# Optimization experiments

Hardware: AMD Instinct MI355X
Metric: run time of the kernel (lower is better)

## Reference

```python
import jax, jax.numpy as jnp
import numpy as np

N_HEADS = 8
TOP_K = 2
EPS = 1e-5


def cross_node(x4, nf, tkv, Wq, bq, Wk, bk, Wv, bv, Wo, bo, gamma, beta, token_mask):
    # x4: [N, BL, 1, D]; nf: [N, BL, K, D]; tkv: [N, K, 1]; token_mask: [N] float (routed subset)
    N, BL, _, D = x4.shape
    K = nf.shape[2]
    H = N_HEADS
    dh = D // H
    nf = nf * tkv[:, None, :, :]  # use_weights: scale neighbors by topk similarity weights
    xf = x4.reshape(N * BL, D)
    nff = nf.reshape(N * BL, K, D)
    q = (xf @ Wq.T + bq).reshape(N * BL, H, dh)
    k = (nff @ Wk.T + bk).reshape(N * BL, K, H, dh)
    v = (nff @ Wv.T + bv).reshape(N * BL, K, H, dh)
    # flash_attn_func math: scaled dot-product over the K neighbors, per head
    scores = jnp.einsum('thd,tkhd->thk', q, k) / jnp.sqrt(jnp.asarray(dh, xf.dtype))
    attn = jax.nn.softmax(scores, axis=-1)
    o = jnp.einsum('thk,tkhd->thd', attn, v).reshape(N * BL, D)
    o = o @ Wo.T + bo
    # masked BatchNorm1d (training-mode batch stats over ONLY the gathered/routed tokens,
    # matching torch where each expert sees just its subset)
    m = jnp.broadcast_to(token_mask[:, None], (N, BL)).reshape(-1, 1)
    cnt = jnp.maximum(m.sum(), 1.0)
    mean = (o * m).sum(0) / cnt
    var = (((o - mean) ** 2) * m).sum(0) / cnt
    o = (o - mean) / jnp.sqrt(var + EPS) * gamma + beta
    return (o + xf).reshape(N, BL, D)


def moe_forward(x, mm, topk_values, Wr, br, eWq, eWk, eWv, eWo, ebq, ebk, ebv, ebo,
                eGamma, eBeta, eW1, eb1, mWq, mWk, mWv, mWo, mbq, mbk, mbv, mbo,
                mGamma, mBeta, mW2, mb2, topk_indices, modality_index):
    N, B, L, D = x.shape
    BL = B * L
    K = topk_indices.shape[1]
    E = Wr.shape[0]
    Mn = mWq.shape[0]
    # neighbor gather: nf[n, b*l, k] = x[topk_indices[n, k], b, l]
    nf = jnp.transpose(x[topk_indices], (0, 2, 3, 1, 4)).reshape(N, BL, K, D)
    x4 = x.reshape(N, BL, 1, D)
    tkv = topk_values.reshape(N, K, 1)
    # router softmax gating
    gate = jax.nn.softmax(mm.reshape(N, D) @ Wr.T + br, axis=-1)  # [N, E]
    _, te = jax.lax.top_k(gate, TOP_K)
    routed = jax.nn.one_hot(te, E, dtype=gate.dtype).sum(1)  # [N, E] 0/1
    f_i = routed.sum(0) / N
    P_i = gate.sum(0) / N
    balance_loss = E * jnp.sum(f_i * P_i)
    # capacity limiting via running cumsum per expert column
    keep = jnp.cumsum(routed, axis=0) <= (N / E)
    rprobs = gate * jnp.where(keep, routed, jnp.zeros_like(routed))
    active = rprobs.sum(-1) > 0  # [N]
    eprobs, eidx = jax.lax.top_k(rprobs, TOP_K)  # [N, TOP_K]
    # expert dispatch/combine (dense-masked equivalent of the per-expert gather/scatter)
    out_tok = jnp.zeros((N, BL, D), x.dtype)
    for i in range(E):
        sel = (eidx == i).any(-1) & active  # tokens gathered for expert i
        mask_f = sel.astype(x.dtype)
        prob_i = (eprobs * (eidx == i)).sum(-1)  # combine weight (0 for capacity-dropped)
        co = cross_node(x4, nf, tkv, eWq[i], ebq[i], eWk[i], ebk[i], eWv[i], ebv[i],
                        eWo[i], ebo[i], eGamma[i], eBeta[i], mask_f)
        co = co @ eW1[i].T + eb1[i]
        out_tok = out_tok + (mask_f * prob_i)[:, None, None] * co
    # modality experts: every token with modality m goes through modality expert m
    mod_out = jnp.zeros_like(out_tok)
    for m in range(Mn):
        mask_f = (modality_index[:, m, :] == 1).any(-1).astype(x.dtype)
        co = cross_node(x4, nf, tkv, mWq[m], mbq[m], mWk[m], mbk[m], mWv[m], mbv[m],
                        mWo[m], mbo[m], mGamma[m], mBeta[m], mask_f)
        co = co @ mW2[m].T + mb2[m]
        mod_out = mod_out + mask_f[:, None, None] * co
    out = (out_tok + mod_out / Mn).reshape(N, B, L, D)
    return out, balance_loss


def setup_inputs():
    key = jax.random.key(0)
    ks = jax.random.split(key, 7)
    N, B, L, D, K, E, Mn = 1024, 2, 8, 128, 16, 4, 4
    s = 1.0 / float(np.sqrt(D))
    inp = {}
    inp['x'] = jax.random.normal(ks[0], (N, B, L, D), jnp.float32)
    inp['mm'] = jax.random.normal(ks[1], (N, 1, D), jnp.float32)
    inp['topk_values'] = jax.random.uniform(ks[2], (N, K), jnp.float32)
    inp['topk_indices'] = jax.random.randint(ks[3], (N, K), 0, N, dtype=jnp.int32)
    inp['modality_index'] = jax.nn.one_hot(
        jax.random.randint(ks[4], (N,), 0, Mn, dtype=jnp.int32), Mn, dtype=jnp.int32
    ).reshape(N, Mn, 1)
    inp['Wr'] = jax.random.normal(ks[5], (E, D), jnp.float32) * s
    inp['br'] = jnp.zeros((E,), jnp.float32)
    kk = jax.random.split(ks[6], 10)
    for j, nm in enumerate(['eWq', 'eWk', 'eWv', 'eWo', 'eW1']):
        inp[nm] = jax.random.normal(kk[j], (E, D, D), jnp.float32) * s
    for j, nm in enumerate(['mWq', 'mWk', 'mWv', 'mWo', 'mW2']):
        inp[nm] = jax.random.normal(kk[5 + j], (Mn, D, D), jnp.float32) * s
    for nm in ['ebq', 'ebk', 'ebv', 'ebo', 'eBeta', 'eb1']:
        inp[nm] = jnp.zeros((E, D), jnp.float32)
    for nm in ['mbq', 'mbk', 'mbv', 'mbo', 'mBeta', 'mb2']:
        inp[nm] = jnp.zeros((Mn, D), jnp.float32)
    inp['eGamma'] = jnp.ones((E, D), jnp.float32)
    inp['mGamma'] = jnp.ones((Mn, D), jnp.float32)
    return inp


def reference(x, mm, topk_values, topk_indices, modality_index, Wr, br,
              eWq, eWk, eWv, eWo, ebq, ebk, ebv, ebo, eGamma, eBeta, eW1, eb1,
              mWq, mWk, mWv, mWo, mbq, mbk, mbv, mbo, mGamma, mBeta, mW2, mb2):
    return moe_forward(x, mm, topk_values, Wr, br, eWq, eWk, eWv, eWo, ebq, ebk, ebv, ebo,
                       eGamma, eBeta, eW1, eb1, mWq, mWk, mWv, mWo, mbq, mbk, mbv, mbo,
                       mGamma, mBeta, mW2, mb2, topk_indices, modality_index)
```

## Files before the change

kernel.cpp:

```cpp
#include <hip/hip_runtime.h>

typedef unsigned short u16;
typedef unsigned int u32;
typedef short short8 __attribute__((ext_vector_type(8)));
typedef float f32x4 __attribute__((ext_vector_type(4)));

#define NTOK 1024
#define TT 16384
#define DD 128
#define EPSV 1e-5f
#define ST 2097152
#define STKV 4194304

__device__ __forceinline__ u16 f2bf(float f) {
    u32 u = __float_as_uint(f);
    u += 0x7fffu + ((u >> 16) & 1u);
    return (u16)(u >> 16);
}
__device__ __forceinline__ u32 pack2(u16 a, u16 b) { return (u32)a | ((u32)b << 16); }
__device__ __forceinline__ void up2(u32 w, float& lo, float& hi) {
    lo = __uint_as_float(w << 16);
    hi = __uint_as_float(w & 0xffff0000u);
}

__global__ __launch_bounds__(1024) void k_prep(const float* __restrict__ x,
        const float* __restrict__ eWq, const float* __restrict__ eWk,
        const float* __restrict__ eWv, const float* __restrict__ eWo, const float* __restrict__ eW1,
        const float* __restrict__ mWq, const float* __restrict__ mWk, const float* __restrict__ mWv,
        const float* __restrict__ mWo, const float* __restrict__ mW2,
        const float* __restrict__ mm, const float* __restrict__ Wr, const float* __restrict__ br,
        const int* __restrict__ modix,
        u16* __restrict__ Xb, u16* __restrict__ Wb,
        float* __restrict__ mask8, float* __restrict__ comb8, float* __restrict__ cnt8,
        float* __restrict__ bnsum, float* __restrict__ bnsq, float* __restrict__ loss) {
    int bid = blockIdx.x; int tid = threadIdx.x;
    if (bid < 256) {
        int i = bid * 1024 + tid;
        const float4* p = (const float4*)x + (size_t)i * 2;
        float4 a = p[0], b = p[1];
        uint4 o;
        o.x = pack2(f2bf(a.x), f2bf(a.y));
        o.y = pack2(f2bf(a.z), f2bf(a.w));
        o.z = pack2(f2bf(b.x), f2bf(b.y));
        o.w = pack2(f2bf(b.z), f2bf(b.w));
        *((uint4*)Xb + i) = o;
        return;
    }
    if (bid < 336) {
        int i = (bid - 256) * 1024 + tid;
        int tns = i >> 13;
        int off = (i & 8191) * 8;
        const float* src;
        switch (tns) {
            case 0: src = eWq; break; case 1: src = eWk; break; case 2: src = eWv; break;
            case 3: src = eWo; break; case 4: src = eW1; break; case 5: src = mWq; break;
            case 6: src = mWk; break; case 7: src = mWv; break; case 8: src = mWo; break;
            default: src = mW2; break;
        }
        const float4* p = (const float4*)(src + off);
        float4 a = p[0], b = p[1];
        uint4 o;
        o.x = pack2(f2bf(a.x), f2bf(a.y));
        o.y = pack2(f2bf(a.z), f2bf(a.w));
        o.z = pack2(f2bf(b.x), f2bf(b.y));
        o.w = pack2(f2bf(b.z), f2bf(b.w));
        *(uint4*)(Wb + tns * 65536 + off) = o;
        return;
    }
    __shared__ int wsum[4][16];
    __shared__ float red[16];
    int n = tid;
    if (n < 16) red[n] = 0.f;
    bnsum[n] = 0.f; bnsq[n] = 0.f;
    float g[4];
    {
        const float4* a = (const float4*)(mm + (size_t)n * DD);
        float4 av[32];
#pragma unroll
        for (int j = 0; j < 32; j++) av[j] = a[j];
#pragma unroll
        for (int e = 0; e < 4; e++) {
            const float4* w = (const float4*)(Wr + (size_t)e * DD);
            float s = 0.f;
#pragma unroll
            for (int j = 0; j < 32; j++) {
                float4 wv = w[j];
                s += av[j].x * wv.x + av[j].y * wv.y + av[j].z * wv.z + av[j].w * wv.w;
            }
            g[e] = s + br[e];
        }
    }
    float mx = -1e30f;
#pragma unroll
    for (int e = 0; e < 4; e++) mx = fmaxf(mx, g[e]);
    float s = 0.f;
#pragma unroll
    for (int e = 0; e < 4; e++) { g[e] = expf(g[e] - mx); s += g[e]; }
    float inv = 1.f / s;
#pragma unroll
    for (int e = 0; e < 4; e++) g[e] *= inv;
    int i0 = 0; float b0 = g[0];
#pragma unroll
    for (int e = 1; e < 4; e++) if (g[e] > b0) { b0 = g[e]; i0 = e; }
    int i1 = -1; float b1v = -1e30f;
#pragma unroll
    for (int e = 0; e < 4; e++) if (e != i0 && g[e] > b1v) { b1v = g[e]; i1 = e; }
    u32 rbits = (1u << i0) | (1u << i1);
    int wav = n >> 6, lane = n & 63;
    unsigned long long lm = (~0ull) >> (63 - lane);
    int pre[4];
#pragma unroll
    for (int e = 0; e < 4; e++) {
        unsigned long long m = __ballot((rbits >> e) & 1u);
        pre[e] = __popcll(m & lm);
        if (lane == 63) wsum[e][wav] = __popcll(m);
    }
    __syncthreads();
    float rp[4]; float rsum = 0.f;
#pragma unroll
    for (int e = 0; e < 4; e++) {
        int off = 0;
        for (int w = 0; w < 16; w++) if (w < wav) off += wsum[e][w];
        bool keep = (off + pre[e]) <= 256;
        rp[e] = (((rbits >> e) & 1u) && keep) ? g[e] : 0.f;
        rsum += rp[e];
    }
    bool active = rsum > 0.f;
    int j0 = 0; float c0 = rp[0];
#pragma unroll
    for (int e = 1; e < 4; e++) if (rp[e] > c0) { c0 = rp[e]; j0 = e; }
    int j1 = -1; float c1 = -1e30f;
#pragma unroll
    for (int e = 0; e < 4; e++) if (e != j0 && rp[e] > c1) { c1 = rp[e]; j1 = e; }
    float vals[16];
#pragma unroll
    for (int e = 0; e < 4; e++) {
        bool sel = active && (e == j0 || e == j1);
        float mf = sel ? 1.f : 0.f;
        mask8[e * NTOK + n] = mf;
        comb8[e * NTOK + n] = rp[e];
        vals[e] = mf;
    }
#pragma unroll
    for (int m = 0; m < 4; m++) {
        float mf = (modix[n * 4 + m] == 1) ? 1.f : 0.f;
        mask8[(4 + m) * NTOK + n] = mf;
        comb8[(4 + m) * NTOK + n] = 0.25f * mf;
        vals[4 + m] = mf;
    }
#pragma unroll
    for (int e = 0; e < 4; e++) vals[8 + e] = ((rbits >> e) & 1u) ? 1.f : 0.f;
#pragma unroll
    for (int e = 0; e < 4; e++) vals[12 + e] = g[e];
#pragma unroll
    for (int q = 0; q < 16; q++) {
        float v = vals[q];
        for (int off = 32; off; off >>= 1) v += __shfl_down(v, off, 64);
        if (lane == 0) atomicAdd(&red[q], v);
    }
    __syncthreads();
    if (n == 0) {
        for (int c = 0; c < 8; c++) cnt8[c] = fmaxf(16.f * red[c], 1.f);
        float l = 0.f;
        for (int e = 0; e < 4; e++) l += (red[8 + e] / 1024.f) * (red[12 + e] / 1024.f);
        loss[0] = 4.f * l;
    }
}

__global__ __launch_bounds__(256) void k_gemm_qkv(const u16* __restrict__ Xb, const u16* __restrict__ Wb,
        const float* __restrict__ ebq, const float* __restrict__ mbq,
        const float* __restrict__ mask8,
        u16* __restrict__ Qb, u16* __restrict__ KVb) {
    __shared__ u16 As[64 * 128];
    __shared__ u16 Bs[128 * 128];
    int tid = threadIdx.x; int bm = blockIdx.x; int c = blockIdx.y;
    int wq = (c < 4) ? c : 20 + (c - 4);
    int wk = (c < 4) ? 4 + c : 24 + (c - 4);
    int wv = (c < 4) ? 8 + c : 28 + (c - 4);
    const u16* Wsl[3] = { Wb + wq * 16384, Wb + wk * 16384, Wb + wv * 16384 };
    const float* bq = (c < 4) ? (ebq + c * 128) : (mbq + (c - 4) * 128);
    const float* maskp = mask8 + c * NTOK;
    bool qact = (maskp[bm * 4] != 0.f) || (maskp[bm * 4 + 1] != 0.f) ||
                (maskp[bm * 4 + 2] != 0.f) || (maskp[bm * 4 + 3] != 0.f);
    u16* Qc  = Qb + (size_t)c * ST;
    u16* KVc = KVb + (size_t)c * STKV;

    const uint4* asrc = (const uint4*)(Xb + (size_t)bm * 8192);
#pragma unroll
    for (int it = 0; it < 4; ++it) {
        int ci = it * 256 + tid;
        uint4 v = asrc[ci];
        int byte = ci * 16; int row = byte >> 8;
        *(uint4*)((char*)As + (byte ^ ((row & 7) << 4))) = v;
    }
    __syncthreads();
    int lane = tid & 63, wid = tid >> 6, lr = lane & 15, lg = lane >> 4;
    short8 a[4];
#pragma unroll
    for (int ks = 0; ks < 4; ++ks) {
        int kk = ks * 64 + lg * 16;
        int arow = wid * 16 + lr;
        a[ks] = *(const short8*)((const char*)As + ((arow * 256 + kk) ^ ((arow & 7) << 4)));
    }
    for (int y = 0; y < 3; ++y) {
        if (y == 0 && !qact) continue;
        const uint4* wsrc = (const uint4*)Wsl[y];
#pragma unroll
        for (int it = 0; it < 8; ++it) {
            int qi = it * 256 + tid;
            uint4 v = wsrc[qi];
            int eo = qi * 8; int row = eo >> 7; int byte = eo * 2;
            *(uint4*)((char*)Bs + (byte ^ ((row & 7) << 4))) = v;
        }
        __syncthreads();
        f32x4 acc[8] = {};
#pragma unroll
        for (int ks = 0; ks < 4; ++ks) {
            int kk = ks * 64 + lg * 16;
#pragma unroll
            for (int nc = 0; nc < 8; ++nc) {
                int brow = nc * 16 + lr;
                short8 b = *(const short8*)((const char*)Bs + ((brow * 256 + kk) ^ ((brow & 7) << 4)));
                acc[nc] = __builtin_amdgcn_mfma_f32_16x16x32_bf16(a[ks], b, acc[nc], 0, 0, 0);
            }
        }
        int row0 = bm * 64 + wid * 16 + lg * 4;
#pragma unroll
        for (int nc = 0; nc < 8; ++nc) {
            int col = nc * 16 + lr;
            float bb = (y == 0) ? bq[col] : 0.f;
#pragma unroll
            for (int r = 0; r < 4; r++) {
                u16 hv = f2bf(acc[nc][r] + bb);
                if (y == 0) Qc[(size_t)(row0 + r) * 128 + col] = hv;
                else KVc[(size_t)(row0 + r) * 256 + (y == 2 ? 128 : 0) + col] = hv;
            }
        }
        __syncthreads();
    }
}

__global__ __launch_bounds__(256) void k_attn(const u16* Qb, const u16* __restrict__ KVb,
        const float* __restrict__ tkv, const int* __restrict__ idx,
        const float* __restrict__ ebk, const float* __restrict__ ebv,
        const float* __restrict__ mbk, const float* __restrict__ mbv,
        const float* __restrict__ mask8, u16* Ob) {
    int bid = blockIdx.x;
    int c = bid & 7, inner = bid >> 3;
    int tid = threadIdx.x;
    int gid = inner * 256 + tid;
    int t = gid >> 3, h = gid & 7;
    int n = __builtin_amdgcn_readfirstlane(t >> 4);
    int bl = t & 15;
    if (mask8[c * NTOK + n] == 0.f) return;
    const int4* ip = (const int4*)(idx + n * 16);
    int4 iv0 = ip[0], iv1 = ip[1], iv2 = ip[2], iv3 = ip[3];
    const float4* tp = (const float4*)(tkv + n * 16);
    float4 tv0 = tp[0], tv1 = tp[1], tv2 = tp[2], tv3 = tp[3];
    const u16* Qc = Qb + (size_t)c * ST;
    const u16* KVc = KVb + (size_t)c * STKV;
    u16* Oc = Ob + (size_t)c * ST;
    const float* bk = (c < 4) ? (ebk + c * 128) : (mbk + (c - 4) * 128);
    const float* bv = (c < 4) ? (ebv + c * 128) : (mbv + (c - 4) * 128);
    float qv[16];
    {
        const uint4* qp = (const uint4*)(Qc + (size_t)t * 128 + h * 16);
        uint4 a = qp[0], b = qp[1];
        up2(a.x, qv[0], qv[1]);   up2(a.y, qv[2], qv[3]);
        up2(a.z, qv[4], qv[5]);   up2(a.w, qv[6], qv[7]);
        up2(b.x, qv[8], qv[9]);   up2(b.y, qv[10], qv[11]);
        up2(b.z, qv[12], qv[13]); up2(b.w, qv[14], qv[15]);
    }
    float qb = 0.f;
#pragma unroll
    for (int i = 0; i < 16; i++) qb += qv[i] * bk[h * 16 + i];
    int gsav[16] = { iv0.x, iv0.y, iv0.z, iv0.w, iv1.x, iv1.y, iv1.z, iv1.w,
                     iv2.x, iv2.y, iv2.z, iv2.w, iv3.x, iv3.y, iv3.z, iv3.w };
    float tsav[16] = { tv0.x, tv0.y, tv0.z, tv0.w, tv1.x, tv1.y, tv1.z, tv1.w,
                       tv2.x, tv2.y, tv2.z, tv2.w, tv3.x, tv3.y, tv3.z, tv3.w };
    float scv[16]; float smax = -1e30f;
#pragma unroll 4
    for (int k = 0; k < 16; k++) {
        const uint4* kp = (const uint4*)(KVc + (size_t)(gsav[k] * 16 + bl) * 256 + h * 16);
        uint4 a = kp[0], b = kp[1];
        float d0 = 0.f, d1 = 0.f, lo, hi;
        up2(a.x, lo, hi); d0 = fmaf(lo, qv[0], d0);  d1 = fmaf(hi, qv[1], d1);
        up2(a.y, lo, hi); d0 = fmaf(lo, qv[2], d0);  d1 = fmaf(hi, qv[3], d1);
        up2(a.z, lo, hi); d0 = fmaf(lo, qv[4], d0);  d1 = fmaf(hi, qv[5], d1);
        up2(a.w, lo, hi); d0 = fmaf(lo, qv[6], d0);  d1 = fmaf(hi, qv[7], d1);
        up2(b.x, lo, hi); d0 = fmaf(lo, qv[8], d0);  d1 = fmaf(hi, qv[9], d1);
        up2(b.y, lo, hi); d0 = fmaf(lo, qv[10], d0); d1 = fmaf(hi, qv[11], d1);
        up2(b.z, lo, hi); d0 = fmaf(lo, qv[12], d0); d1 = fmaf(hi, qv[13], d1);
        up2(b.w, lo, hi); d0 = fmaf(lo, qv[14], d0); d1 = fmaf(hi, qv[15], d1);
        float sv = 0.25f * (tsav[k] * (d0 + d1) + qb);
        scv[k] = sv; smax = fmaxf(smax, sv);
    }
    float sum = 0.f;
#pragma unroll
    for (int k = 0; k < 16; k++) { scv[k] = __expf(scv[k] - smax); sum += scv[k]; }
    float inv = 1.f / sum;
    float o[16];
#pragma unroll
    for (int i = 0; i < 16; i++) o[i] = 0.f;
#pragma unroll 4
    for (int k = 0; k < 16; k++) {
        const uint4* vp = (const uint4*)(KVc + (size_t)(gsav[k] * 16 + bl) * 256 + 128 + h * 16);
        uint4 a = vp[0], b = vp[1];
        float cc = scv[k] * inv * tsav[k];
        float lo, hi;
        up2(a.x, lo, hi); o[0] = fmaf(lo, cc, o[0]);   o[1] = fmaf(hi, cc, o[1]);
        up2(a.y, lo, hi); o[2] = fmaf(lo, cc, o[2]);   o[3] = fmaf(hi, cc, o[3]);
        up2(a.z, lo, hi); o[4] = fmaf(lo, cc, o[4]);   o[5] = fmaf(hi, cc, o[5]);
        up2(a.w, lo, hi); o[6] = fmaf(lo, cc, o[6]);   o[7] = fmaf(hi, cc, o[7]);
        up2(b.x, lo, hi); o[8] = fmaf(lo, cc, o[8]);   o[9] = fmaf(hi, cc, o[9]);
        up2(b.y, lo, hi); o[10] = fmaf(lo, cc, o[10]); o[11] = fmaf(hi, cc, o[11]);
        up2(b.z, lo, hi); o[12] = fmaf(lo, cc, o[12]); o[13] = fmaf(hi, cc, o[13]);
        up2(b.w, lo, hi); o[14] = fmaf(lo, cc, o[14]); o[15] = fmaf(hi, cc, o[15]);
    }
#pragma unroll
    for (int i = 0; i < 16; i++) o[i] += bv[h * 16 + i];
    uint4 s0, s1;
    s0.x = pack2(f2bf(o[0]), f2bf(o[1]));  s0.y = pack2(f2bf(o[2]), f2bf(o[3]));
    s0.z = pack2(f2bf(o[4]), f2bf(o[5]));  s0.w = pack2(f2bf(o[6]), f2bf(o[7]));
    s1.x = pack2(f2bf(o[8]), f2bf(o[9]));  s1.y = pack2(f2bf(o[10]), f2bf(o[11]));
    s1.z = pack2(f2bf(o[12]), f2bf(o[13])); s1.w = pack2(f2bf(o[14]), f2bf(o[15]));
    uint4* op = (uint4*)(Oc + (size_t)t * 128 + h * 16);
    op[0] = s0; op[1] = s1;
}

__global__ __launch_bounds__(256) void k_gemm_o(const u16* __restrict__ Ab, const u16* __restrict__ Wb,
        const float* __restrict__ ebo, const float* __restrict__ mbo,
        u16* __restrict__ O2, const float* __restrict__ mask8,
        float* __restrict__ bnsum, float* __restrict__ bnsq) {
    __shared__ u16 As[64 * 128];
    __shared__ u16 Bs[128 * 128];
    __shared__ float ssum[128], ssq[128];
    int tid = threadIdx.x; int bm = blockIdx.x; int c = blockIdx.y;
    const float* maskp = mask8 + c * NTOK;
    if (maskp[bm * 4] == 0.f && maskp[bm * 4 + 1] == 0.f &&
        maskp[bm * 4 + 2] == 0.f && maskp[bm * 4 + 3] == 0.f) return;
    int wo = (c < 4) ? 12 + c : 32 + (c - 4);
    const u16* Wp = Wb + wo * 16384;
    const float* bo = (c < 4) ? (ebo + c * 128) : (mbo + (c - 4) * 128);
    if (tid < 128) { ssum[tid] = 0.f; ssq[tid] = 0.f; }
    const uint4* asrc = (const uint4*)(Ab + (size_t)c * ST + (size_t)bm * 8192);
#pragma unroll
    for (int it = 0; it < 4; ++it) {
        int ci = it * 256 + tid;
        uint4 v = asrc[ci];
        int byte = ci * 16; int row = byte >> 8;
        *(uint4*)((char*)As + (byte ^ ((row & 7) << 4))) = v;
    }
    const uint4* wsrc = (const uint4*)Wp;
#pragma unroll
    for (int it = 0; it < 8; ++it) {
        int qi = it * 256 + tid;
        uint4 v = wsrc[qi];
        int eo = qi * 8; int row = eo >> 7; int byte = eo * 2;
        *(uint4*)((char*)Bs + (byte ^ ((row & 7) << 4))) = v;
    }
    __syncthreads();
    int lane = tid & 63, wid = tid >> 6, lr = lane & 15, lg = lane >> 4;
    f32x4 acc[8] = {};
#pragma unroll
    for (int ks = 0; ks < 4; ++ks) {
        int kk = ks * 64 + lg * 16;
        int arow = wid * 16 + lr;
        short8 a = *(const short8*)((const char*)As + ((arow * 256 + kk) ^ ((arow & 7) << 4)));
#pragma unroll
        for (int nc = 0; nc < 8; ++nc) {
            int brow = nc * 16 + lr;
            short8 b = *(const short8*)((const char*)Bs + ((brow * 256 + kk) ^ ((brow & 7) << 4)));
            acc[nc] = __builtin_amdgcn_mfma_f32_16x16x32_bf16(a, b, acc[nc], 0, 0, 0);
        }
    }
    int nidx = bm * 4 + wid;
    float mk = maskp[nidx];
    int row0 = bm * 64 + wid * 16 + lg * 4;
    u16* O2c = O2 + (size_t)c * ST;
    float ps[8], pq[8];
#pragma unroll
    for (int nc = 0; nc < 8; ++nc) {
        int col = nc * 16 + lr;
        float bb = bo[col];
        float sv = 0.f, qv = 0.f;
#pragma unroll
        for (int r = 0; r < 4; r++) {
            float v = acc[nc][r] + bb;
            if (mk != 0.f) O2c[(size_t)(row0 + r) * 128 + col] = f2bf(v);
            sv += v; qv += v * v;
        }
        ps[nc] = sv * mk; pq[nc] = qv * mk;
    }
#pragma unroll
    for (int nc = 0; nc < 8; ++nc) {
        ps[nc] += __shfl_xor(ps[nc], 16, 64); ps[nc] += __shfl_xor(ps[nc], 32, 64);
        pq[nc] += __shfl_xor(pq[nc], 16, 64); pq[nc] += __shfl_xor(pq[nc], 32, 64);
    }
    if (lane < 16) {
#pragma unroll
        for (int nc = 0; nc < 8; ++nc) {
            atomicAdd(&ssum[nc * 16 + lane], ps[nc]);
            atomicAdd(&ssq[nc * 16 + lane], pq[nc]);
        }
    }
    __syncthreads();
    if (tid < 128) { atomicAdd(&bnsum[c * 128 + tid], ssum[tid]); atomicAdd(&bnsq[c * 128 + tid], ssq[tid]); }
}

__global__ __launch_bounds__(512) void k_gemm_w1(const u16* __restrict__ O2, const u16* __restrict__ Xb,
        const u16* __restrict__ Wb, const float* __restrict__ eb1, const float* __restrict__ mb2,
        const float* __restrict__ eGamma, const float* __restrict__ mGamma,
        const float* __restrict__ eBeta, const float* __restrict__ mBeta,
        const float* __restrict__ comb8, const float* __restrict__ cnt8,
        const float* __restrict__ bnsum, const float* __restrict__ bnsq,
        float* __restrict__ out) {
    __shared__ u16 As[64 * 128];
    __shared__ u16 Bs[128 * 128];
    __shared__ float scall[8][128], shall[8][128];
    int tid = threadIdx.x; int bm = blockIdx.x;
#pragma unroll
    for (int j = 0; j < 2; ++j) {
        int id = j * 512 + tid;
        int c = id >> 7, d = id & 127;
        float cnt = cnt8[c];
        float mean = bnsum[c * 128 + d] / cnt;
        float var = bnsq[c * 128 + d] / cnt - mean * mean;
        float rs = rsqrtf(var + EPSV);
        const float* ga = (c < 4) ? (eGamma + c * 128) : (mGamma + (c - 4) * 128);
        const float* be = (c < 4) ? (eBeta + c * 128) : (mBeta + (c - 4) * 128);
        float gg = ga[d];
        scall[c][d] = rs * gg;
        shall[c][d] = be[d] - mean * rs * gg;
    }
    __syncthreads();
    int lane = tid & 63, wid = tid >> 6, lr = lane & 15, lg = lane >> 4;
    int wm = wid & 3, wn = wid >> 2;
    f32x4 acc[4] = {};
    const uint4* xsrc = (const uint4*)(Xb + (size_t)bm * 8192);
    for (int c = 0; c < 8; ++c) {
        float wc4[4];
        wc4[0] = comb8[c * NTOK + bm * 4];     wc4[1] = comb8[c * NTOK + bm * 4 + 1];
        wc4[2] = comb8[c * NTOK + bm * 4 + 2]; wc4[3] = comb8[c * NTOK + bm * 4 + 3];
        if (wc4[0] == 0.f && wc4[1] == 0.f && wc4[2] == 0.f && wc4[3] == 0.f) continue;
        int wsl = (c < 4) ? 16 + c : 36 + (c - 4);
        const u16* Wp = Wb + wsl * 16384;
        const uint4* osrc = (const uint4*)(O2 + (size_t)c * ST + (size_t)bm * 8192);
#pragma unroll
        for (int it = 0; it < 2; ++it) {
            int qi = it * 512 + tid;
            int eo = qi * 8; int row = eo >> 7; int cb = eo & 127;
            float wc = wc4[row >> 4];
            uint4 ov = osrc[qi]; uint4 xv = xsrc[qi];
            float olo, ohi, xlo, xhi;
            uint4 hh;
            up2(ov.x, olo, ohi); up2(xv.x, xlo, xhi);
            hh.x = pack2(f2bf((olo * scall[c][cb] + shall[c][cb] + xlo) * wc),
                         f2bf((ohi * scall[c][cb + 1] + shall[c][cb + 1] + xhi) * wc));
            up2(ov.y, olo, ohi); up2(xv.y, xlo, xhi);
            hh.y = pack2(f2bf((olo * scall[c][cb + 2] + shall[c][cb + 2] + xlo) * wc),
                         f2bf((ohi * scall[c][cb + 3] + shall[c][cb + 3] + xhi) * wc));
            up2(ov.z, olo, ohi); up2(xv.z, xlo, xhi);
            hh.z = pack2(f2bf((olo * scall[c][cb + 4] + shall[c][cb + 4] + xlo) * wc),
                         f2bf((ohi * scall[c][cb + 5] + shall[c][cb + 5] + xhi) * wc));
            up2(ov.w, olo, ohi); up2(xv.w, xlo, xhi);
            hh.w = pack2(f2bf((olo * scall[c][cb + 6] + shall[c][cb + 6] + xlo) * wc),
                         f2bf((ohi * scall[c][cb + 7] + shall[c][cb + 7] + xhi) * wc));
            *(uint4*)((char*)As + ((eo * 2) ^ ((row & 7) << 4))) = hh;
        }
        const uint4* wsrc = (const uint4*)Wp;
#pragma unroll
        for (int it = 0; it < 4; ++it) {
            int qi = it * 512 + tid;
            uint4 v = wsrc[qi];
            int eo = qi * 8; int row = eo >> 7; int byte = eo * 2;
            *(uint4*)((char*)Bs + (byte ^ ((row & 7) << 4))) = v;
        }
        __syncthreads();
#pragma unroll
        for (int ks = 0; ks < 4; ++ks) {
            int kk = ks * 64 + lg * 16;
            int arow = wm * 16 + lr;
            short8 a = *(const short8*)((const char*)As + ((arow * 256 + kk) ^ ((arow & 7) << 4)));
#pragma unroll
            for (int nc = 0; nc < 4; ++nc) {
                int brow = wn * 64 + nc * 16 + lr;
                short8 b = *(const short8*)((const char*)Bs + ((brow * 256 + kk) ^ ((brow & 7) << 4)));
                acc[nc] = __builtin_amdgcn_mfma_f32_16x16x32_bf16(a, b, acc[nc], 0, 0, 0);
            }
        }
        __syncthreads();
    }
    int nidx = bm * 4 + wm;
    int row0 = bm * 64 + wm * 16 + lg * 4;
    float wc8[8];
#pragma unroll
    for (int c = 0; c < 8; ++c) wc8[c] = comb8[c * NTOK + nidx];
#pragma unroll
    for (int nc = 0; nc < 4; ++nc) {
        int col = wn * 64 + nc * 16 + lr;
        float bias = 0.f;
#pragma unroll
        for (int c = 0; c < 8; ++c) {
            const float* b1 = (c < 4) ? (eb1 + c * 128) : (mb2 + (c - 4) * 128);
            bias += wc8[c] * b1[col];
        }
#pragma unroll
        for (int r = 0; r < 4; r++)
            out[(size_t)(row0 + r) * 128 + col] = acc[nc][r] + bias;
    }
}

extern "C" void kernel_launch(void* const* d_in, const int* in_sizes, int n_in,
                              void* d_out, int out_size, void* d_ws, size_t ws_size,
                              hipStream_t stream) {
    (void)in_sizes; (void)n_in; (void)ws_size; (void)out_size;
    const float* x    = (const float*)d_in[0];
    const float* mm   = (const float*)d_in[1];
    const float* tkv  = (const float*)d_in[2];
    const int*   idx  = (const int*)d_in[3];
    const int*   modi = (const int*)d_in[4];
    const float* Wr   = (const float*)d_in[5];
    const float* br   = (const float*)d_in[6];
    const float* eWq = (const float*)d_in[7],  *eWk = (const float*)d_in[8],  *eWv = (const float*)d_in[9];
    const float* eWo = (const float*)d_in[10], *eW1 = (const float*)d_in[11];
    const float* mWq = (const float*)d_in[12], *mWk = (const float*)d_in[13], *mWv = (const float*)d_in[14];
    const float* mWo = (const float*)d_in[15], *mW2 = (const float*)d_in[16];
    const float* ebq = (const float*)d_in[17], *ebk = (const float*)d_in[18], *ebv = (const float*)d_in[19];
    const float* ebo = (const float*)d_in[20], *eBeta = (const float*)d_in[21], *eb1 = (const float*)d_in[22];
    const float* mbq = (const float*)d_in[23], *mbk = (const float*)d_in[24], *mbv = (const float*)d_in[25];
    const float* mbo = (const float*)d_in[26], *mBeta = (const float*)d_in[27], *mb2 = (const float*)d_in[28];
    const float* eGamma = (const float*)d_in[29], *mGamma = (const float*)d_in[30];
    float* out = (float*)d_out;

    char* wsb = (char*)d_ws;
    const size_t MB = 1024 * 1024;
    u16* Xb  = (u16*)wsb;
    u16* Wb  = (u16*)(wsb + 4 * MB);
    u16* Qb  = (u16*)(wsb + 8 * MB);
    u16* KVb = (u16*)(wsb + 40 * MB);
    u16* O2  = (u16*)(wsb + 104 * MB);
    float* comb8 = (float*)(wsb + 136 * MB);
    float* mask8 = comb8 + 8192;
    float* cnt8  = mask8 + 8192;
    float* bnsum = cnt8 + 16;
    float* bnsq  = bnsum + 1024;

    k_prep<<<337, 1024, 0, stream>>>(x, eWq, eWk, eWv, eWo, eW1, mWq, mWk, mWv, mWo, mW2,
                                     mm, Wr, br, modi, Xb, Wb,
                                     mask8, comb8, cnt8, bnsum, bnsq, out + (size_t)TT * DD);
    k_gemm_qkv<<<dim3(256, 8), 256, 0, stream>>>(Xb, Wb, ebq, mbq, mask8, Qb, KVb);
    k_attn<<<4096, 256, 0, stream>>>(Qb, KVb, tkv, idx, ebk, ebv, mbk, mbv, mask8, Qb);
    k_gemm_o<<<dim3(256, 8), 256, 0, stream>>>(Qb, Wb, ebo, mbo, O2, mask8, bnsum, bnsq);
    k_gemm_w1<<<256, 512, 0, stream>>>(O2, Xb, Wb, eb1, mb2, eGamma, mGamma, eBeta, mBeta,
                                       comb8, cnt8, bnsum, bnsq, out);
}
```

Before: 131.0 us.

## Shrink prep blocks to 256 threads and fuse attention into online softmax

```diff
diff --git a/kernel.cpp b/kernel.cpp
--- a/kernel.cpp
+++ b/kernel.cpp
@@ -23,7 +23,7 @@
     hi = __uint_as_float(w & 0xffff0000u);
 }
 
-__global__ __launch_bounds__(1024) void k_prep(const float* __restrict__ x,
+__global__ __launch_bounds__(256) void k_prep(const float* __restrict__ x,
         const float* __restrict__ eWq, const float* __restrict__ eWk,
         const float* __restrict__ eWv, const float* __restrict__ eWo, const float* __restrict__ eW1,
         const float* __restrict__ mWq, const float* __restrict__ mWk, const float* __restrict__ mWv,
@@ -34,8 +34,8 @@
         float* __restrict__ mask8, float* __restrict__ comb8, float* __restrict__ cnt8,
         float* __restrict__ bnsum, float* __restrict__ bnsq, float* __restrict__ loss) {
     int bid = blockIdx.x; int tid = threadIdx.x;
-    if (bid < 256) {
-        int i = bid * 1024 + tid;
+    if (bid < 1024) {
+        int i = bid * 256 + tid;
         const float4* p = (const float4*)x + (size_t)i * 2;
         float4 a = p[0], b = p[1];
         uint4 o;
@@ -46,8 +46,8 @@
         *((uint4*)Xb + i) = o;
         return;
     }
-    if (bid < 336) {
-        int i = (bid - 256) * 1024 + tid;
+    if (bid < 1344) {
+        int i = (bid - 1024) * 256 + tid;
         int tns = i >> 13;
         int off = (i & 8191) * 8;
         const float* src;
@@ -67,99 +67,125 @@
         *(uint4*)(Wb + tns * 65536 + off) = o;
         return;
     }
-    __shared__ int wsum[4][16];
+    __shared__ int wsumLDS[4][4];
     __shared__ float red[16];
-    int n = tid;
-    if (n < 16) red[n] = 0.f;
-    bnsum[n] = 0.f; bnsq[n] = 0.f;
-    float g[4];
-    {
-        const float4* a = (const float4*)(mm + (size_t)n * DD);
-        float4 av[32];
-#pragma unroll
-        for (int j = 0; j < 32; j++) av[j] = a[j];
+    int lane = tid & 63, wav = tid >> 6;
+    if (tid < 16) red[tid] = 0.f;
+#pragma unroll
+    for (int q = 0; q < 4; q++) { bnsum[tid + q * 256] = 0.f; bnsq[tid + q * 256] = 0.f; }
+    float g[4][4];
+    u32 rb[4];
+#pragma unroll
+    for (int j = 0; j < 4; j++) {
+        int n = tid * 4 + j;
+        const float4* a  = (const float4*)(mm + (size_t)n * DD);
+        const float4* w0 = (const float4*)(Wr);
+        const float4* w1p = (const float4*)(Wr + DD);
+        const float4* w2 = (const float4*)(Wr + 2 * DD);
+        const float4* w3 = (const float4*)(Wr + 3 * DD);
+        float s0 = 0.f, s1 = 0.f, s2 = 0.f, s3 = 0.f;
+#pragma unroll
+        for (int jj = 0; jj < 32; jj++) {
+            float4 av = a[jj];
+            float4 v0 = w0[jj], v1 = w1p[jj], v2 = w2[jj], v3 = w3[jj];
+            s0 += av.x * v0.x + av.y * v0.y + av.z * v0.z + av.w * v0.w;
+            s1 += av.x * v1.x + av.y * v1.y + av.z * v1.z + av.w * v1.w;
+            s2 += av.x * v2.x + av.y * v2.y + av.z * v2.z + av.w * v2.w;
+            s3 += av.x * v3.x + av.y * v3.y + av.z * v3.z + av.w * v3.w;
+        }
+        float gg[4] = { s0 + br[0], s1 + br[1], s2 + br[2], s3 + br[3] };
+        float mx = fmaxf(fmaxf(gg[0], gg[1]), fmaxf(gg[2], gg[3]));
+        float ss = 0.f;
+#pragma unroll
+        for (int e = 0; e < 4; e++) { gg[e] = expf(gg[e] - mx); ss += gg[e]; }
+        float inv = 1.f / ss;
+#pragma unroll
+        for (int e = 0; e < 4; e++) gg[e] *= inv;
+        int i0 = 0; float b0 = gg[0];
+#pragma unroll
+        for (int e = 1; e < 4; e++) if (gg[e] > b0) { b0 = gg[e]; i0 = e; }
+        int i1 = -1; float b1v = -1e30f;
+#pragma unroll
+        for (int e = 0; e < 4; e++) if (e != i0 && gg[e] > b1v) { b1v = gg[e]; i1 = e; }
+        rb[j] = (1u << i0) | (1u << i1);
+#pragma unroll
+        for (int e = 0; e < 4; e++) g[j][e] = gg[e];
+    }
+    int cnt[4], loc[4][4];
+#pragma unroll
+    for (int e = 0; e < 4; e++) {
+        int cc = 0;
+#pragma unroll
+        for (int j = 0; j < 4; j++) { cc += (rb[j] >> e) & 1; loc[e][j] = cc; }
+        cnt[e] = cc;
+    }
+    int base[4];
+#pragma unroll
+    for (int e = 0; e < 4; e++) {
+        int v = cnt[e];
+        for (int off = 1; off < 64; off <<= 1) {
+            int y = __shfl_up(v, off, 64);
+            if (lane >= off) v += y;
+        }
+        if (lane == 63) wsumLDS[e][wav] = v;
+        base[e] = v - cnt[e];
+    }
+    __syncthreads();
+#pragma unroll
+    for (int e = 0; e < 4; e++) {
+        int o = 0;
+        for (int w = 0; w < 4; w++) if (w < wav) o += wsumLDS[e][w];
+        base[e] += o;
+    }
+    float sums[16];
+#pragma unroll
+    for (int q = 0; q < 16; q++) sums[q] = 0.f;
+#pragma unroll
+    for (int j = 0; j < 4; j++) {
+        int n = tid * 4 + j;
+        float rp[4]; float rsum = 0.f;
 #pragma unroll
         for (int e = 0; e < 4; e++) {
-            const float4* w = (const float4*)(Wr + (size_t)e * DD);
-            float s = 0.f;
-#pragma unroll
-            for (int j = 0; j < 32; j++) {
-                float4 wv = w[j];
-                s += av[j].x * wv.x + av[j].y * wv.y + av[j].z * wv.z + av[j].w * wv.w;
-            }
-            g[e] = s + br[e];
-        }
-    }
-    float mx = -1e30f;
-#pragma unroll
-    for (int e = 0; e < 4; e++) mx = fmaxf(mx, g[e]);
-    float s = 0.f;
-#pragma unroll
-    for (int e = 0; e < 4; e++) { g[e] = expf(g[e] - mx); s += g[e]; }
-    float inv = 1.f / s;
-#pragma unroll
-    for (int e = 0; e < 4; e++) g[e] *= inv;
-    int i0 = 0; float b0 = g[0];
-#pragma unroll
-    for (int e = 1; e < 4; e++) if (g[e] > b0) { b0 = g[e]; i0 = e; }
-    int i1 = -1; float b1v = -1e30f;
-#pragma unroll
-    for (int e = 0; e < 4; e++) if (e != i0 && g[e] > b1v) { b1v = g[e]; i1 = e; }
-    u32 rbits = (1u << i0) | (1u << i1);
-    int wav = n >> 6, lane = n & 63;
-    unsigned long long lm = (~0ull) >> (63 - lane);
-    int pre[4];
-#pragma unroll
-    for (int e = 0; e < 4; e++) {
-        unsigned long long m = __ballot((rbits >> e) & 1u);
-        pre[e] = __popcll(m & lm);
-        if (lane == 63) wsum[e][wav] = __popcll(m);
-    }
-    __syncthreads();
-    float rp[4]; float rsum = 0.f;
-#pragma unroll
-    for (int e = 0; e < 4; e++) {
-        int off = 0;
-        for (int w = 0; w < 16; w++) if (w < wav) off += wsum[e][w];
-        bool keep = (off + pre[e]) <= 256;
-        rp[e] = (((rbits >> e) & 1u) && keep) ? g[e] : 0.f;
-        rsum += rp[e];
-    }
-    bool active = rsum > 0.f;
-    int j0 = 0; float c0 = rp[0];
-#pragma unroll
-    for (int e = 1; e < 4; e++) if (rp[e] > c0) { c0 = rp[e]; j0 = e; }
-    int j1 = -1; float c1 = -1e30f;
-#pragma unroll
-    for (int e = 0; e < 4; e++) if (e != j0 && rp[e] > c1) { c1 = rp[e]; j1 = e; }
-    float vals[16];
-#pragma unroll
-    for (int e = 0; e < 4; e++) {
-        bool sel = active && (e == j0 || e == j1);
-        float mf = sel ? 1.f : 0.f;
-        mask8[e * NTOK + n] = mf;
-        comb8[e * NTOK + n] = rp[e];
-        vals[e] = mf;
-    }
-#pragma unroll
-    for (int m = 0; m < 4; m++) {
-        float mf = (modix[n * 4 + m] == 1) ? 1.f : 0.f;
-        mask8[(4 + m) * NTOK + n] = mf;
-        comb8[(4 + m) * NTOK + n] = 0.25f * mf;
-        vals[4 + m] = mf;
-    }
-#pragma unroll
-    for (int e = 0; e < 4; e++) vals[8 + e] = ((rbits >> e) & 1u) ? 1.f : 0.f;
-#pragma unroll
-    for (int e = 0; e < 4; e++) vals[12 + e] = g[e];
+            int bit = (rb[j] >> e) & 1;
+            bool keep = (base[e] + loc[e][j]) <= 256;
+            rp[e] = (bit && keep) ? g[j][e] : 0.f;
+            rsum += rp[e];
+        }
+        bool active = rsum > 0.f;
+        int j0 = 0; float c0 = rp[0];
+#pragma unroll
+        for (int e = 1; e < 4; e++) if (rp[e] > c0) { c0 = rp[e]; j0 = e; }
+        int j1 = -1; float c1 = -1e30f;
+#pragma unroll
+        for (int e = 0; e < 4; e++) if (e != j0 && rp[e] > c1) { c1 = rp[e]; j1 = e; }
+#pragma unroll
+        for (int e = 0; e < 4; e++) {
+            bool sel = active && (e == j0 || e == j1);
+            float mf = sel ? 1.f : 0.f;
+            mask8[e * NTOK + n] = mf;
+            comb8[e * NTOK + n] = rp[e];
+            sums[e] += mf;
+        }
+#pragma unroll
+        for (int mmod = 0; mmod < 4; mmod++) {
+            float mf = (modix[n * 4 + mmod] == 1) ? 1.f : 0.f;
+            mask8[(4 + mmod) * NTOK + n] = mf;
+            comb8[(4 + mmod) * NTOK + n] = 0.25f * mf;
+            sums[4 + mmod] += mf;
+        }
+#pragma unroll
+        for (int e = 0; e < 4; e++) sums[8 + e] += (float)((rb[j] >> e) & 1);
+#pragma unroll
+        for (int e = 0; e < 4; e++) sums[12 + e] += g[j][e];
+    }
 #pragma unroll
     for (int q = 0; q < 16; q++) {
-        float v = vals[q];
+        float v = sums[q];
         for (int off = 32; off; off >>= 1) v += __shfl_down(v, off, 64);
         if (lane == 0) atomicAdd(&red[q], v);
     }
     __syncthreads();
-    if (n == 0) {
+    if (tid == 0) {
         for (int c = 0; c < 8; c++) cnt8[c] = fmaxf(16.f * red[c], 1.f);
         float l = 0.f;
         for (int e = 0; e < 4; e++) l += (red[8 + e] / 1024.f) * (red[12 + e] / 1024.f);
@@ -278,47 +304,45 @@
                      iv2.x, iv2.y, iv2.z, iv2.w, iv3.x, iv3.y, iv3.z, iv3.w };
     float tsav[16] = { tv0.x, tv0.y, tv0.z, tv0.w, tv1.x, tv1.y, tv1.z, tv1.w,
                        tv2.x, tv2.y, tv2.z, tv2.w, tv3.x, tv3.y, tv3.z, tv3.w };
-    float scv[16]; float smax = -1e30f;
-#pragma unroll 4
+    float m = -1e30f, l = 0.f;
+    float o[16];
+#pragma unroll
+    for (int i = 0; i < 16; i++) o[i] = 0.f;
+#pragma unroll 2
     for (int k = 0; k < 16; k++) {
-        const uint4* kp = (const uint4*)(KVc + (size_t)(gsav[k] * 16 + bl) * 256 + h * 16);
-        uint4 a = kp[0], b = kp[1];
+        const u16* basep = KVc + (size_t)(gsav[k] * 16 + bl) * 256 + h * 16;
+        const uint4* kp = (const uint4*)basep;
+        const uint4* vp = (const uint4*)(basep + 128);
+        uint4 ka = kp[0], kb2 = kp[1];
+        uint4 va = vp[0], vb2 = vp[1];
         float d0 = 0.f, d1 = 0.f, lo, hi;
-        up2(a.x, lo, hi); d0 = fmaf(lo, qv[0], d0);  d1 = fmaf(hi, qv[1], d1);
-        up2(a.y, lo, hi); d0 = fmaf(lo, qv[2], d0);  d1 = fmaf(hi, qv[3], d1);
-        up2(a.z, lo, hi); d0 = fmaf(lo, qv[4], d0);  d1 = fmaf(hi, qv[5], d1);
-        up2(a.w, lo, hi); d0 = fmaf(lo, qv[6], d0);  d1 = fmaf(hi, qv[7], d1);
-        up2(b.x, lo, hi); d0 = fmaf(lo, qv[8], d0);  d1 = fmaf(hi, qv[9], d1);
-        up2(b.y, lo, hi); d0 = fmaf(lo, qv[10], d0); d1 = fmaf(hi, qv[11], d1);
-        up2(b.z, lo, hi); d0 = fmaf(lo, qv[12], d0); d1 = fmaf(hi, qv[13], d1);
-        up2(b.w, lo, hi); d0 = fmaf(lo, qv[14], d0); d1 = fmaf(hi, qv[15], d1);
+        up2(ka.x, lo, hi);  d0 = fmaf(lo, qv[0], d0);  d1 = fmaf(hi, qv[1], d1);
+        up2(ka.y, lo, hi);  d0 = fmaf(lo, qv[2], d0);  d1 = fmaf(hi, qv[3], d1);
+        up2(ka.z, lo, hi);  d0 = fmaf(lo, qv[4], d0);  d1 = fmaf(hi, qv[5], d1);
+        up2(ka.w, lo, hi);  d0 = fmaf(lo, qv[6], d0);  d1 = fmaf(hi, qv[7], d1);
+        up2(kb2.x, lo, hi); d0 = fmaf(lo, qv[8], d0);  d1 = fmaf(hi, qv[9], d1);
+        up2(kb2.y, lo, hi); d0 = fmaf(lo, qv[10], d0); d1 = fmaf(hi, qv[11], d1);
+        up2(kb2.z, lo, hi); d0 = fmaf(lo, qv[12], d0); d1 = fmaf(hi, qv[13], d1);
+        up2(kb2.w, lo, hi); d0 = fmaf(lo, qv[14], d0); d1 = fmaf(hi, qv[15], d1);
         float sv = 0.25f * (tsav[k] * (d0 + d1) + qb);
-        scv[k] = sv; smax = fmaxf(smax, sv);
-    }
-    float sum = 0.f;
-#pragma unroll
-    for (int k = 0; k < 16; k++) { scv[k] = __expf(scv[k] - smax); sum += scv[k]; }
-    float inv = 1.f / sum;
-    float o[16];
-#pragma unroll
-    for (int i = 0; i < 16; i++) o[i] = 0.f;
-#pragma unroll 4
-    for (int k = 0; k < 16; k++) {
-        const uint4* vp = (const uint4*)(KVc + (size_t)(gsav[k] * 16 + bl) * 256 + 128 + h * 16);
-        uint4 a = vp[0], b = vp[1];
-        float cc = scv[k] * inv * tsav[k];
-        float lo, hi;
-        up2(a.x, lo, hi); o[0] = fmaf(lo, cc, o[0]);   o[1] = fmaf(hi, cc, o[1]);
-        up2(a.y, lo, hi); o[2] = fmaf(lo, cc, o[2]);   o[3] = fmaf(hi, cc, o[3]);
-        up2(a.z, lo, hi); o[4] = fmaf(lo, cc, o[4]);   o[5] = fmaf(hi, cc, o[5]);
-        up2(a.w, lo, hi); o[6] = fmaf(lo, cc, o[6]);   o[7] = fmaf(hi, cc, o[7]);
-        up2(b.x, lo, hi); o[8] = fmaf(lo, cc, o[8]);   o[9] = fmaf(hi, cc, o[9]);
-        up2(b.y, lo, hi); o[10] = fmaf(lo, cc, o[10]); o[11] = fmaf(hi, cc, o[11]);
-        up2(b.z, lo, hi); o[12] = fmaf(lo, cc, o[12]); o[13] = fmaf(hi, cc, o[13]);
-        up2(b.w, lo, hi); o[14] = fmaf(lo, cc, o[14]); o[15] = fmaf(hi, cc, o[15]);
-    }
-#pragma unroll
-    for (int i = 0; i < 16; i++) o[i] += bv[h * 16 + i];
+        float nm = fmaxf(m, sv);
+        float scale = __expf(m - nm);
+        float e = __expf(sv - nm);
+        m = nm;
+        l = fmaf(l, scale, e);
+        float cc = e * tsav[k];
+        up2(va.x, lo, hi);  o[0] = fmaf(o[0], scale, cc * lo);   o[1] = fmaf(o[1], scale, cc * hi);
+        up2(va.y, lo, hi);  o[2] = fmaf(o[2], scale, cc * lo);   o[3] = fmaf(o[3], scale, cc * hi);
+        up2(va.z, lo, hi);  o[4] = fmaf(o[4], scale, cc * lo);   o[5] = fmaf(o[5], scale, cc * hi);
+        up2(va.w, lo, hi);  o[6] = fmaf(o[6], scale, cc * lo);   o[7] = fmaf(o[7], scale, cc * hi);
+        up2(vb2.x, lo, hi); o[8] = fmaf(o[8], scale, cc * lo);   o[9] = fmaf(o[9], scale, cc * hi);
+        up2(vb2.y, lo, hi); o[10] = fmaf(o[10], scale, cc * lo); o[11] = fmaf(o[11], scale, cc * hi);
+        up2(vb2.z, lo, hi); o[12] = fmaf(o[12], scale, cc * lo); o[13] = fmaf(o[13], scale, cc * hi);
+        up2(vb2.w, lo, hi); o[14] = fmaf(o[14], scale, cc * lo); o[15] = fmaf(o[15], scale, cc * hi);
+    }
+    float inv = 1.f / l;
+#pragma unroll
+    for (int i = 0; i < 16; i++) o[i] = fmaf(o[i], inv, bv[h * 16 + i]);
     uint4 s0, s1;
     s0.x = pack2(f2bf(o[0]), f2bf(o[1]));  s0.y = pack2(f2bf(o[2]), f2bf(o[3]));
     s0.z = pack2(f2bf(o[4]), f2bf(o[5]));  s0.w = pack2(f2bf(o[6]), f2bf(o[7]));
@@ -546,7 +570,7 @@
     float* bnsum = cnt8 + 16;
     float* bnsq  = bnsum + 1024;
 
-    k_prep<<<337, 1024, 0, stream>>>(x, eWq, eWk, eWv, eWo, eW1, mWq, mWk, mWv, mWo, mW2,
+    k_prep<<<1345, 256, 0, stream>>>(x, eWq, eWk, eWv, eWo, eW1, mWq, mWk, mWv, mWo, mW2,
                                      mm, Wr, br, modi, Xb, Wb,
                                      mask8, comb8, cnt8, bnsum, bnsq, out + (size_t)TT * DD);
     k_gemm_qkv<<<dim3(256, 8), 256, 0, stream>>>(Xb, Wb, ebq, mbq, mask8, Qb, KVb);
```

Measured after the change: 132.6 us. No clear change (+1.3%).
